# Optimization experiments

Measured on AMD Instinct MI355X. Metric: run time of the kernel, lower is better.

The kernel has to match this reference:

```python
import jax, jax.numpy as jnp
import numpy as np


def _extract_patches(x):
    # x: [B,28,28] -> [B,196,4]; patch elems [x[r,c], x[r,c+1], x[r+1,c], x[r+1,c+1]]
    B = x.shape[0]
    p = x.reshape(B, 14, 2, 14, 2)           # [B, r, dr, c, dc]
    p = jnp.transpose(p, (0, 1, 3, 2, 4))    # [B, r, c, dr, dc]
    return p.reshape(B, 196, 4)


def _simulate(patches, params):
    # All gates are single-qubit and the state starts at |0000>, so the 4-wire
    # state stays a product state: simulate each qubit as a complex 2-vector
    # (a, b), vectorized over [B, P=196, W=4].
    half = patches * 0.5
    a = jnp.cos(half).astype(jnp.complex64)   # amplitude of |0>
    b = jnp.sin(half).astype(jnp.complex64)   # amplitude of |1>  (RY encoding of |0>)
    depth = params.shape[0]
    for d in range(depth):  # small fixed structural loop
        rz1 = params[d, :, 0]
        ry = params[d, :, 1]
        rz2 = params[d, :, 2]
        # RZ(t) = diag(e^{-it/2}, e^{it/2})
        ph1 = jnp.exp(-0.5j * rz1.astype(jnp.complex64))  # [W], broadcasts over B,P
        a = a * ph1
        b = b * jnp.conj(ph1)
        # RY(t) = [[cos(t/2), -sin(t/2)], [sin(t/2), cos(t/2)]]
        c = jnp.cos(ry * 0.5).astype(jnp.complex64)
        s = jnp.sin(ry * 0.5).astype(jnp.complex64)
        a, b = c * a - s * b, s * a + c * b
        ph2 = jnp.exp(-0.5j * rz2.astype(jnp.complex64))
        a = a * ph2
        b = b * jnp.conj(ph2)
    # <Z> per wire for a product state
    z = (jnp.real(a * jnp.conj(a)) - jnp.real(b * jnp.conj(b))).astype(jnp.float32)  # [B,196,4]
    return z.reshape(z.shape[0], -1)  # [B, 784], patch-major then wire order (matches torch cat)


def setup_inputs() -> dict:
    key = jax.random.key(0)
    k1, k2, k3, k4 = jax.random.split(key, 4)
    B, depth = 8192, 4
    x = jax.random.uniform(k1, (B, 1, 28, 28), dtype=jnp.float32)
    params = jax.random.normal(k2, (depth, 4, 3), dtype=jnp.float32)
    w = jax.random.normal(k3, (10, 784), dtype=jnp.float32) * (1.0 / np.sqrt(784.0))
    bias = jax.random.normal(k4, (10,), dtype=jnp.float32) * 0.01
    return {"x": x, "params": params, "w": w, "bias": bias}


def reference(x, params, w, bias):
    B = x.shape[0]
    patches = _extract_patches(x.reshape(B, 28, 28))
    feats = _simulate(patches, params)          # [B, 784]
    logits = feats @ w.T + bias                 # [B, 10]
    return jax.nn.log_softmax(logits, axis=-1)
```

## Files before the change

kernel.cpp:

```cpp
#include <hip/hip_runtime.h>
#include <math.h>

struct c2 { float re, im; };
__device__ inline c2 cmul(c2 a, c2 b){ return {a.re*b.re - a.im*b.im, a.re*b.im + a.im*b.re}; }
__device__ inline c2 cadd(c2 a, c2 b){ return {a.re+b.re, a.im+b.im}; }

__global__ __launch_bounds__(256) void quanv_kernel(
    const float* __restrict__ x, const float* __restrict__ params,
    const float* __restrict__ w, const float* __restrict__ bias,
    float* __restrict__ out, int Bn)
{
    __shared__ __align__(16) float tab[832 * 12];
    __shared__ float wls[4][40];

    const int tid  = threadIdx.x;
    const int lane = tid & 63;
    const int wid  = tid >> 6;

    float Aq[4], Bq[4];
    #pragma unroll
    for (int q = 0; q < 4; ++q) {
        c2 m00 = {1.f, 0.f}, m01 = {0.f, 0.f}, m10 = {0.f, 0.f}, m11 = {1.f, 0.f};
        #pragma unroll
        for (int d = 0; d < 4; ++d) {
            float rz1 = params[(d * 4 + q) * 3 + 0];
            float ry  = params[(d * 4 + q) * 3 + 1];
            float rz2 = params[(d * 4 + q) * 3 + 2];
            float c  = __cosf(0.5f * ry),  s  = __sinf(0.5f * ry);
            c2 ph1  = { __cosf(0.5f * rz1), -__sinf(0.5f * rz1) };
            c2 ph1c = { ph1.re, -ph1.im };
            c2 ph2  = { __cosf(0.5f * rz2), -__sinf(0.5f * rz2) };
            c2 ph2c = { ph2.re, -ph2.im };
            c2 d00 = cmul(ph2,  { c * ph1.re,  c * ph1.im });
            c2 d01 = cmul(ph2,  {-s * ph1c.re, -s * ph1c.im});
            c2 d10 = cmul(ph2c, { s * ph1.re,  s * ph1.im });
            c2 d11 = cmul(ph2c, { c * ph1c.re, c * ph1c.im});
            c2 n00 = cadd(cmul(d00, m00), cmul(d01, m10));
            c2 n01 = cadd(cmul(d00, m01), cmul(d01, m11));
            c2 n10 = cadd(cmul(d10, m00), cmul(d11, m10));
            c2 n11 = cadd(cmul(d10, m01), cmul(d11, m11));
            m00 = n00; m01 = n01; m10 = n10; m11 = n11;
        }
        float n00 = m00.re*m00.re + m00.im*m00.im;
        float n10 = m10.re*m10.re + m10.im*m10.im;
        float n01 = m01.re*m01.re + m01.im*m01.im;
        float n11 = m11.re*m11.re + m11.im*m11.im;
        Aq[q] = 0.5f * (n00 - n10 - n01 + n11);
        Bq[q] = (m00.re*m01.re + m00.im*m01.im) - (m10.re*m11.re + m10.im*m11.im);
    }

    for (int m = tid; m < 832; m += 256) {
        if (m < 784) {
            int r = m / 28, col = m - 28 * r;
            int q = ((r & 1) << 1) | (col & 1);
            tab[m * 12 + 0] = Aq[q];
            tab[m * 12 + 1] = Bq[q];
        } else {
            #pragma unroll
            for (int k = 0; k < 12; ++k) tab[m * 12 + k] = 0.f;
        }
    }
    for (int idx = tid; idx < 7840; idx += 256) {
        int c = idx / 784, f = idx - 784 * c;
        int p = f >> 2, q = f & 3;
        int pi = p / 14, pj = p - 14 * pi;
        int r = 2 * pi + (q >> 1), col = 2 * pj + (q & 1);
        int m = r * 28 + col;
        tab[m * 12 + 2 + c] = w[idx];
    }
    __syncthreads();

    const float4* tab4 = (const float4*)tab;

    int b0 = blockIdx.x * 16 + wid * 4;
    const float* xr[4];
    #pragma unroll
    for (int s = 0; s < 4; ++s) {
        int bs = b0 + s; if (bs > Bn - 1) bs = Bn - 1;
        xr[s] = x + (size_t)bs * 784;
    }

    float acc[4][10];
    #pragma unroll
    for (int s = 0; s < 4; ++s)
        #pragma unroll
        for (int c = 0; c < 10; ++c) acc[s][c] = 0.f;

    for (int it = 0; it < 13; ++it) {
        int m = it * 64 + lane;
        int mm = m < 784 ? m : 783;
        float4 t0 = tab4[m * 3 + 0];
        float4 t1 = tab4[m * 3 + 1];
        float4 t2 = tab4[m * 3 + 2];
        float al = t0.x, be = t0.y;
        float wg[10] = {t0.z, t0.w, t1.x, t1.y, t1.z, t1.w, t2.x, t2.y, t2.z, t2.w};
        float xv[4];
        #pragma unroll
        for (int s = 0; s < 4; ++s) xv[s] = xr[s][mm];
        #pragma unroll
        for (int s = 0; s < 4; ++s) {
            float cs = __cosf(xv[s]);
            float sn = __sinf(xv[s]);
            float z  = al * cs + be * sn;
            #pragma unroll
            for (int c = 0; c < 10; ++c) acc[s][c] = fmaf(z, wg[c], acc[s][c]);
        }
    }

    #pragma unroll
    for (int s = 0; s < 4; ++s) {
        #pragma unroll
        for (int c = 0; c < 10; ++c) {
            float v = acc[s][c];
            v += __shfl_xor(v, 32, 64);
            v += __shfl_xor(v, 16, 64);
            v += __shfl_xor(v,  8, 64);
            v += __shfl_xor(v,  4, 64);
            v += __shfl_xor(v,  2, 64);
            v += __shfl_xor(v,  1, 64);
            if (lane == 0) wls[wid][s * 10 + c] = v;
        }
    }
    __syncthreads();

    if (lane < 40) {
        int s = lane / 10, c = lane - 10 * s;
        const float* L = &wls[wid][s * 10];
        float mx = -1e30f;
        #pragma unroll
        for (int k = 0; k < 10; ++k) { float v = L[k] + bias[k]; mx = fmaxf(mx, v); }
        float sum = 0.f;
        #pragma unroll
        for (int k = 0; k < 10; ++k) sum += __expf(L[k] + bias[k] - mx);
        float lse = mx + __logf(sum);
        int b = b0 + s;
        if (b < Bn) out[b * 10 + c] = (L[c] + bias[c]) - lse;
    }
}

extern "C" void kernel_launch(void* const* d_in, const int* in_sizes, int n_in,
                              void* d_out, int out_size, void* d_ws, size_t ws_size,
                              hipStream_t stream) {
    const float* x      = (const float*)d_in[0];
    const float* params = (const float*)d_in[1];
    const float* w      = (const float*)d_in[2];
    const float* bias   = (const float*)d_in[3];
    float* out = (float*)d_out;
    int Bn = in_sizes[0] / 784;
    int grid = (Bn + 15) / 16;
    quanv_kernel<<<grid, 256, 0, stream>>>(x, params, w, bias, out, Bn);
}
```

Measured before the change: 89.20 us.

## Split into table, per-sample partial-dot and reduce kernels with global table

Builds the per-pixel alpha/beta and weight table once in a small kernel and stores it in workspace, instead of every block recomputing the SU(2) products and scattering all weights into shared memory. The main kernel assigns one sample per lane and splits the 196 pixel chunks across 16 blocks, reading x as float4 and reading the table with wave-uniform addresses. It writes partial logits to workspace, and a third kernel sums them and applies log-softmax. In exchange it adds two extra launches, a round trip of partial sums through global memory, and strided per-lane x reads.

```diff
diff --git a/kernel.cpp b/kernel.cpp
--- a/kernel.cpp
+++ b/kernel.cpp
@@ -1,23 +1,15 @@
 #include <hip/hip_runtime.h>
 #include <math.h>
+
+#define NCHUNK 208
+#define NPB 16
+#define CHPW 13
 
 struct c2 { float re, im; };
 __device__ inline c2 cmul(c2 a, c2 b){ return {a.re*b.re - a.im*b.im, a.re*b.im + a.im*b.re}; }
 __device__ inline c2 cadd(c2 a, c2 b){ return {a.re+b.re, a.im+b.im}; }
 
-__global__ __launch_bounds__(256) void quanv_kernel(
-    const float* __restrict__ x, const float* __restrict__ params,
-    const float* __restrict__ w, const float* __restrict__ bias,
-    float* __restrict__ out, int Bn)
-{
-    __shared__ __align__(16) float tab[832 * 12];
-    __shared__ float wls[4][40];
-
-    const int tid  = threadIdx.x;
-    const int lane = tid & 63;
-    const int wid  = tid >> 6;
-
-    float Aq[4], Bq[4];
+__device__ inline void su2_alpha_beta(const float* __restrict__ params, float* Aq, float* Bq) {
     #pragma unroll
     for (int q = 0; q < 4; ++q) {
         c2 m00 = {1.f, 0.f}, m01 = {0.f, 0.f}, m10 = {0.f, 0.f}, m11 = {1.f, 0.f};
@@ -48,94 +40,119 @@
         Aq[q] = 0.5f * (n00 - n10 - n01 + n11);
         Bq[q] = (m00.re*m01.re + m00.im*m01.im) - (m10.re*m11.re + m10.im*m11.im);
     }
+}
 
-    for (int m = tid; m < 832; m += 256) {
-        if (m < 784) {
-            int r = m / 28, col = m - 28 * r;
-            int q = ((r & 1) << 1) | (col & 1);
-            tab[m * 12 + 0] = Aq[q];
-            tab[m * 12 + 1] = Bq[q];
-        } else {
-            #pragma unroll
-            for (int k = 0; k < 12; ++k) tab[m * 12 + k] = 0.f;
+__global__ __launch_bounds__(64) void k1_table(
+    const float* __restrict__ params, const float* __restrict__ w,
+    float4* __restrict__ tab4)
+{
+    float Aq[4], Bq[4];
+    su2_alpha_beta(params, Aq, Bq);
+    int t = threadIdx.x, b = blockIdx.x;
+    #pragma unroll
+    for (int k = 0; k < 3; ++k) {
+        int j    = t + 64 * k;
+        int ch   = b * 16 + (j / 12);
+        int slot = j % 12;
+        float v[4];
+        #pragma unroll
+        for (int e = 0; e < 4; ++e) {
+            int px = ch * 4 + e;
+            float val = 0.f;
+            if (px < 784) {
+                int r = px / 28, col = px - 28 * r;
+                int q = ((r & 1) << 1) | (col & 1);
+                if (slot == 0)      val = Aq[q];
+                else if (slot == 1) val = Bq[q];
+                else {
+                    int pi = r >> 1, pj = col >> 1;
+                    int f  = (pi * 14 + pj) * 4 + q;
+                    val = w[(slot - 2) * 784 + f];
+                }
+            }
+            v[e] = val;
         }
+        tab4[ch * 12 + slot] = make_float4(v[0], v[1], v[2], v[3]);
     }
-    for (int idx = tid; idx < 7840; idx += 256) {
-        int c = idx / 784, f = idx - 784 * c;
-        int p = f >> 2, q = f & 3;
-        int pi = p / 14, pj = p - 14 * pi;
-        int r = 2 * pi + (q >> 1), col = 2 * pj + (q & 1);
-        int m = r * 28 + col;
-        tab[m * 12 + 2 + c] = w[idx];
-    }
-    __syncthreads();
+}
 
-    const float4* tab4 = (const float4*)tab;
+__global__ __launch_bounds__(64) void k2_main(
+    const float* __restrict__ x, const float4* __restrict__ tab4,
+    float* __restrict__ partial, int Bn)
+{
+    int bid  = blockIdx.x;
+    int pb   = bid & (NPB - 1);
+    int sg   = bid >> 4;
+    int lane = threadIdx.x;
+    int s    = sg * 64 + lane;
+    if (s >= Bn) s = Bn - 1;
 
-    int b0 = blockIdx.x * 16 + wid * 4;
-    const float* xr[4];
+    const float4* x4 = (const float4*)x;
+    size_t xbase = (size_t)s * 196;
+    int ch0 = pb * CHPW;
+
+    float acc[10];
     #pragma unroll
-    for (int s = 0; s < 4; ++s) {
-        int bs = b0 + s; if (bs > Bn - 1) bs = Bn - 1;
-        xr[s] = x + (size_t)bs * 784;
-    }
+    for (int c = 0; c < 10; ++c) acc[c] = 0.f;
 
-    float acc[4][10];
     #pragma unroll
-    for (int s = 0; s < 4; ++s)
+    for (int i = 0; i < CHPW; ++i) {
+        int ch  = ch0 + i;
+        int chx = ch < 196 ? ch : 195;
+        float4 xv = x4[xbase + chx];
+        float4 al = tab4[ch * 12 + 0];
+        float4 be = tab4[ch * 12 + 1];
+        float z0 = fmaf(al.x, __cosf(xv.x), be.x * __sinf(xv.x));
+        float z1 = fmaf(al.y, __cosf(xv.y), be.y * __sinf(xv.y));
+        float z2 = fmaf(al.z, __cosf(xv.z), be.z * __sinf(xv.z));
+        float z3 = fmaf(al.w, __cosf(xv.w), be.w * __sinf(xv.w));
         #pragma unroll
-        for (int c = 0; c < 10; ++c) acc[s][c] = 0.f;
-
-    for (int it = 0; it < 13; ++it) {
-        int m = it * 64 + lane;
-        int mm = m < 784 ? m : 783;
-        float4 t0 = tab4[m * 3 + 0];
-        float4 t1 = tab4[m * 3 + 1];
-        float4 t2 = tab4[m * 3 + 2];
-        float al = t0.x, be = t0.y;
-        float wg[10] = {t0.z, t0.w, t1.x, t1.y, t1.z, t1.w, t2.x, t2.y, t2.z, t2.w};
-        float xv[4];
-        #pragma unroll
-        for (int s = 0; s < 4; ++s) xv[s] = xr[s][mm];
-        #pragma unroll
-        for (int s = 0; s < 4; ++s) {
-            float cs = __cosf(xv[s]);
-            float sn = __sinf(xv[s]);
-            float z  = al * cs + be * sn;
-            #pragma unroll
-            for (int c = 0; c < 10; ++c) acc[s][c] = fmaf(z, wg[c], acc[s][c]);
+        for (int cl = 0; cl < 10; ++cl) {
+            float4 wv = tab4[ch * 12 + 2 + cl];
+            acc[cl] = fmaf(z0, wv.x, acc[cl]);
+            acc[cl] = fmaf(z1, wv.y, acc[cl]);
+            acc[cl] = fmaf(z2, wv.z, acc[cl]);
+            acc[cl] = fmaf(z3, wv.w, acc[cl]);
         }
     }
 
+    int so = sg * 64 + lane;
+    if (so < Bn) {
+        float2* p2 = (float2*)(partial + ((size_t)pb * Bn + so) * 10);
+        #pragma unroll
+        for (int c = 0; c < 5; ++c) p2[c] = make_float2(acc[2*c], acc[2*c+1]);
+    }
+}
+
+__global__ __launch_bounds__(256) void k3_reduce(
+    const float* __restrict__ partial, const float* __restrict__ bias,
+    float* __restrict__ out, int Bn)
+{
+    int s = blockIdx.x * 256 + threadIdx.x;
+    if (s >= Bn) return;
+    float l[10];
     #pragma unroll
-    for (int s = 0; s < 4; ++s) {
+    for (int c = 0; c < 10; ++c) l[c] = bias[c];
+    #pragma unroll
+    for (int pb = 0; pb < NPB; ++pb) {
+        const float2* p2 = (const float2*)(partial + ((size_t)pb * Bn + s) * 10);
         #pragma unroll
-        for (int c = 0; c < 10; ++c) {
-            float v = acc[s][c];
-            v += __shfl_xor(v, 32, 64);
-            v += __shfl_xor(v, 16, 64);
-            v += __shfl_xor(v,  8, 64);
-            v += __shfl_xor(v,  4, 64);
-            v += __shfl_xor(v,  2, 64);
-            v += __shfl_xor(v,  1, 64);
-            if (lane == 0) wls[wid][s * 10 + c] = v;
+        for (int c = 0; c < 5; ++c) {
+            float2 v = p2[c];
+            l[2*c]   += v.x;
+            l[2*c+1] += v.y;
         }
     }
-    __syncthreads();
-
-    if (lane < 40) {
-        int s = lane / 10, c = lane - 10 * s;
-        const float* L = &wls[wid][s * 10];
-        float mx = -1e30f;
-        #pragma unroll
-        for (int k = 0; k < 10; ++k) { float v = L[k] + bias[k]; mx = fmaxf(mx, v); }
-        float sum = 0.f;
-        #pragma unroll
-        for (int k = 0; k < 10; ++k) sum += __expf(L[k] + bias[k] - mx);
-        float lse = mx + __logf(sum);
-        int b = b0 + s;
-        if (b < Bn) out[b * 10 + c] = (L[c] + bias[c]) - lse;
-    }
+    float mx = l[0];
+    #pragma unroll
+    for (int c = 1; c < 10; ++c) mx = fmaxf(mx, l[c]);
+    float sum = 0.f;
+    #pragma unroll
+    for (int c = 0; c < 10; ++c) sum += __expf(l[c] - mx);
+    float lse = mx + __logf(sum);
+    float2* o2 = (float2*)(out + (size_t)s * 10);
+    #pragma unroll
+    for (int c = 0; c < 5; ++c) o2[c] = make_float2(l[2*c] - lse, l[2*c+1] - lse);
 }
 
 extern "C" void kernel_launch(void* const* d_in, const int* in_sizes, int n_in,
@@ -147,6 +164,14 @@
     const float* bias   = (const float*)d_in[3];
     float* out = (float*)d_out;
     int Bn = in_sizes[0] / 784;
-    int grid = (Bn + 15) / 16;
-    quanv_kernel<<<grid, 256, 0, stream>>>(x, params, w, bias, out, Bn);
+
+    float* tab     = (float*)d_ws;
+    float* partial = (float*)((char*)d_ws + 40960);
+
+    k1_table<<<13, 64, 0, stream>>>(params, w, (float4*)tab);
+
+    int nsg = (Bn + 63) / 64;
+    k2_main<<<nsg * NPB, 64, 0, stream>>>(x, (const float4*)tab, partial, Bn);
+
+    k3_reduce<<<(Bn + 255) / 256, 256, 0, stream>>>(partial, bias, out, Bn);
 }
```

After: 92.84 us. 4.1% more time.

## Precompute coefficient/weight table in separate kernel and vectorize x loads

Applied to the files above, without the earlier changes.

Moves the per-block SU(2) coefficient and permuted weight table construction into a small prologue kernel that writes a structure-of-arrays float4 table to workspace. Each main block then copies that table into LDS with coalesced float4 loads instead of recomputing trig and doing scattered weight gathers. The main loop reads x as float4 (4 pixels per lane, 4 iterations instead of 13). This adds a second kernel launch and relies on the workspace being large enough for the table.

```diff
diff --git a/kernel.cpp b/kernel.cpp
--- a/kernel.cpp
+++ b/kernel.cpp
@@ -1,23 +1,13 @@
 #include <hip/hip_runtime.h>
 #include <math.h>
+
+#define NCH 256
 
 struct c2 { float re, im; };
 __device__ inline c2 cmul(c2 a, c2 b){ return {a.re*b.re - a.im*b.im, a.re*b.im + a.im*b.re}; }
 __device__ inline c2 cadd(c2 a, c2 b){ return {a.re+b.re, a.im+b.im}; }
 
-__global__ __launch_bounds__(256) void quanv_kernel(
-    const float* __restrict__ x, const float* __restrict__ params,
-    const float* __restrict__ w, const float* __restrict__ bias,
-    float* __restrict__ out, int Bn)
-{
-    __shared__ __align__(16) float tab[832 * 12];
-    __shared__ float wls[4][40];
-
-    const int tid  = threadIdx.x;
-    const int lane = tid & 63;
-    const int wid  = tid >> 6;
-
-    float Aq[4], Bq[4];
+__device__ inline void su2_alpha_beta(const float* __restrict__ params, float* Aq, float* Bq) {
     #pragma unroll
     for (int q = 0; q < 4; ++q) {
         c2 m00 = {1.f, 0.f}, m01 = {0.f, 0.f}, m10 = {0.f, 0.f}, m11 = {1.f, 0.f};
@@ -48,83 +38,114 @@
         Aq[q] = 0.5f * (n00 - n10 - n01 + n11);
         Bq[q] = (m00.re*m01.re + m00.im*m01.im) - (m10.re*m11.re + m10.im*m11.im);
     }
+}
 
-    for (int m = tid; m < 832; m += 256) {
+__global__ __launch_bounds__(256) void k0_table(
+    const float* __restrict__ params, const float* __restrict__ w,
+    float4* __restrict__ tab4)
+{
+    int slot = blockIdx.x;
+    int c    = threadIdx.x;
+    float Aq[4], Bq[4];
+    if (slot < 2) su2_alpha_beta(params, Aq, Bq);
+    float v[4];
+    #pragma unroll
+    for (int e = 0; e < 4; ++e) {
+        int m = c * 4 + e;
+        float val = 0.f;
         if (m < 784) {
             int r = m / 28, col = m - 28 * r;
             int q = ((r & 1) << 1) | (col & 1);
-            tab[m * 12 + 0] = Aq[q];
-            tab[m * 12 + 1] = Bq[q];
-        } else {
-            #pragma unroll
-            for (int k = 0; k < 12; ++k) tab[m * 12 + k] = 0.f;
+            if (slot == 0)      val = Aq[q];
+            else if (slot == 1) val = Bq[q];
+            else {
+                int f = ((r >> 1) * 14 + (col >> 1)) * 4 + q;
+                val = w[(slot - 2) * 784 + f];
+            }
         }
+        v[e] = val;
     }
-    for (int idx = tid; idx < 7840; idx += 256) {
-        int c = idx / 784, f = idx - 784 * c;
-        int p = f >> 2, q = f & 3;
-        int pi = p / 14, pj = p - 14 * pi;
-        int r = 2 * pi + (q >> 1), col = 2 * pj + (q & 1);
-        int m = r * 28 + col;
-        tab[m * 12 + 2 + c] = w[idx];
-    }
+    tab4[slot * NCH + c] = make_float4(v[0], v[1], v[2], v[3]);
+}
+
+__global__ __launch_bounds__(256) void k_main(
+    const float* __restrict__ x, const float4* __restrict__ tab4,
+    const float* __restrict__ bias, float* __restrict__ out, int Bn)
+{
+    __shared__ __align__(16) float4 lds4[12 * NCH];
+    __shared__ float wls[4][40];
+
+    const int tid  = threadIdx.x;
+    const int lane = tid & 63;
+    const int wid  = tid >> 6;
+
+    #pragma unroll
+    for (int k = 0; k < 12; ++k) lds4[tid + 256 * k] = tab4[tid + 256 * k];
     __syncthreads();
 
-    const float4* tab4 = (const float4*)tab;
-
+    const float4* x4 = (const float4*)x;
     int b0 = blockIdx.x * 16 + wid * 4;
-    const float* xr[4];
+    size_t xb[4];
     #pragma unroll
     for (int s = 0; s < 4; ++s) {
         int bs = b0 + s; if (bs > Bn - 1) bs = Bn - 1;
-        xr[s] = x + (size_t)bs * 784;
+        xb[s] = (size_t)bs * 196;
     }
 
     float acc[4][10];
     #pragma unroll
     for (int s = 0; s < 4; ++s)
         #pragma unroll
-        for (int c = 0; c < 10; ++c) acc[s][c] = 0.f;
+        for (int cl = 0; cl < 10; ++cl) acc[s][cl] = 0.f;
 
-    for (int it = 0; it < 13; ++it) {
-        int m = it * 64 + lane;
-        int mm = m < 784 ? m : 783;
-        float4 t0 = tab4[m * 3 + 0];
-        float4 t1 = tab4[m * 3 + 1];
-        float4 t2 = tab4[m * 3 + 2];
-        float al = t0.x, be = t0.y;
-        float wg[10] = {t0.z, t0.w, t1.x, t1.y, t1.z, t1.w, t2.x, t2.y, t2.z, t2.w};
-        float xv[4];
+    #pragma unroll
+    for (int it = 0; it < 4; ++it) {
+        int c  = it * 64 + lane;
+        int cx = c < 196 ? c : 195;
+        float4 xv[4];
         #pragma unroll
-        for (int s = 0; s < 4; ++s) xv[s] = xr[s][mm];
+        for (int s = 0; s < 4; ++s) xv[s] = x4[xb[s] + cx];
+        float4 al = lds4[c];
+        float4 be = lds4[NCH + c];
+        float z[4][4];
         #pragma unroll
         for (int s = 0; s < 4; ++s) {
-            float cs = __cosf(xv[s]);
-            float sn = __sinf(xv[s]);
-            float z  = al * cs + be * sn;
+            z[s][0] = fmaf(al.x, __cosf(xv[s].x), be.x * __sinf(xv[s].x));
+            z[s][1] = fmaf(al.y, __cosf(xv[s].y), be.y * __sinf(xv[s].y));
+            z[s][2] = fmaf(al.z, __cosf(xv[s].z), be.z * __sinf(xv[s].z));
+            z[s][3] = fmaf(al.w, __cosf(xv[s].w), be.w * __sinf(xv[s].w));
+        }
+        #pragma unroll
+        for (int cl = 0; cl < 10; ++cl) {
+            float4 wv = lds4[(2 + cl) * NCH + c];
             #pragma unroll
-            for (int c = 0; c < 10; ++c) acc[s][c] = fmaf(z, wg[c], acc[s][c]);
+            for (int s = 0; s < 4; ++s) {
+                acc[s][cl] = fmaf(z[s][0], wv.x, acc[s][cl]);
+                acc[s][cl] = fmaf(z[s][1], wv.y, acc[s][cl]);
+                acc[s][cl] = fmaf(z[s][2], wv.z, acc[s][cl]);
+                acc[s][cl] = fmaf(z[s][3], wv.w, acc[s][cl]);
+            }
         }
     }
 
     #pragma unroll
     for (int s = 0; s < 4; ++s) {
         #pragma unroll
-        for (int c = 0; c < 10; ++c) {
-            float v = acc[s][c];
+        for (int cl = 0; cl < 10; ++cl) {
+            float v = acc[s][cl];
             v += __shfl_xor(v, 32, 64);
             v += __shfl_xor(v, 16, 64);
             v += __shfl_xor(v,  8, 64);
             v += __shfl_xor(v,  4, 64);
             v += __shfl_xor(v,  2, 64);
             v += __shfl_xor(v,  1, 64);
-            if (lane == 0) wls[wid][s * 10 + c] = v;
+            if (lane == 0) wls[wid][s * 10 + cl] = v;
         }
     }
     __syncthreads();
 
     if (lane < 40) {
-        int s = lane / 10, c = lane - 10 * s;
+        int s = lane / 10, cl = lane - 10 * s;
         const float* L = &wls[wid][s * 10];
         float mx = -1e30f;
         #pragma unroll
@@ -134,7 +155,7 @@
         for (int k = 0; k < 10; ++k) sum += __expf(L[k] + bias[k] - mx);
         float lse = mx + __logf(sum);
         int b = b0 + s;
-        if (b < Bn) out[b * 10 + c] = (L[c] + bias[c]) - lse;
+        if (b < Bn) out[b * 10 + cl] = (L[cl] + bias[cl]) - lse;
     }
 }
 
@@ -147,6 +168,9 @@
     const float* bias   = (const float*)d_in[3];
     float* out = (float*)d_out;
     int Bn = in_sizes[0] / 784;
-    int grid = (Bn + 15) / 16;
-    quanv_kernel<<<grid, 256, 0, stream>>>(x, params, w, bias, out, Bn);
+
+    float4* tab4 = (float4*)d_ws;
+
+    k0_table<<<12, 256, 0, stream>>>(params, w, tab4);
+    k_main<<<(Bn + 15) / 16, 256, 0, stream>>>(x, tab4, bias, out, Bn);
 }
```

New measurement: 97.21 us. +9.0%, slower.
